# Optimization experiments

Hardware: AMD Instinct MI355X
Metric: run time of the kernel (lower is better)

Reference implementation:

```python
import jax, jax.numpy as jnp
import numpy as np

N = 50000       # num nodes
E = 600000      # num edges
IN = 128        # in_channels
H = 4           # heads
C = 32          # out_channels per head
B = 3           # num bends (Bezier control points)
NEG_SLOPE = 0.2


def setup_inputs() -> dict:
    key = jax.random.key(0)
    ks = jax.random.split(key, 6)
    x = jax.random.normal(ks[0], (N, IN), dtype=jnp.float32)
    edge_index = jax.random.randint(ks[1], (2, E), 0, N)
    # Bezier coefficients at t=0.5 for a 3-point curve: [0.25, 0.5, 0.25]
    coeffs_t = jnp.array([0.25, 0.5, 0.25], dtype=jnp.float32)
    glorot_w = float(np.sqrt(2.0) * np.sqrt(6.0 / (H * C + IN)))
    glorot_a = float(np.sqrt(2.0) * np.sqrt(6.0 / (1 + C)))
    lin_weight = jax.random.uniform(ks[2], (B, H * C, IN), jnp.float32, -glorot_w, glorot_w)
    lin_bias = jnp.zeros((B, H * C), dtype=jnp.float32)
    att_src = jax.random.uniform(ks[3], (B, 1, H, C), jnp.float32, -glorot_a, glorot_a)
    att_dst = jax.random.uniform(ks[4], (B, 1, H, C), jnp.float32, -glorot_a, glorot_a)
    return {"x": x, "edge_index": edge_index, "coeffs_t": coeffs_t,
            "lin_weight": lin_weight, "lin_bias": lin_bias,
            "att_src": att_src, "att_dst": att_dst}


def reference(x, edge_index, coeffs_t, lin_weight, lin_bias, att_src, att_dst):
    # Bezier parameter interpolation: weighted sum over bends
    W = jnp.einsum('b,boi->oi', coeffs_t, lin_weight)      # [H*C, IN]
    bias = jnp.einsum('b,bo->o', coeffs_t, lin_bias)       # [H*C]
    a_src = jnp.einsum('b,bqhc->qhc', coeffs_t, att_src)   # [1,H,C]
    a_dst = jnp.einsum('b,bqhc->qhc', coeffs_t, att_dst)   # [1,H,C]

    n = x.shape[0]
    xt = (x @ W.T + bias).reshape(n, H, C)                 # [N,H,C]
    alpha_src = jnp.sum(xt * a_src, axis=-1)               # [N,H]
    alpha_dst = jnp.sum(xt * a_dst, axis=-1)               # [N,H]

    row, col = edge_index[0], edge_index[1]
    alpha = alpha_src[row] + alpha_dst[col]                # [E,H]
    alpha = jax.nn.leaky_relu(alpha, NEG_SLOPE)

    # scatter-softmax over incoming edges of each target node (col)
    amax = jax.ops.segment_max(alpha, col, num_segments=n)  # [N,H]
    ex = jnp.exp(alpha - amax[col])                         # [E,H]
    denom = jax.ops.segment_sum(ex, col, num_segments=n)    # [N,H]
    alpha = ex / (denom[col] + 1e-16)                       # [E,H]

    # weighted neighbor aggregation (edge-parallel segment reduction)
    msg = xt[row] * alpha[..., None]                        # [E,H,C]
    out = jax.ops.segment_sum(msg, col, num_segments=n)     # [N,H,C]
    return out.reshape(n, H * C)                            # concat=True
```

## Files before the change

### kernel.cpp

```cpp
#include <hip/hip_runtime.h>
#include <hip/hip_bf16.h>

#define GAT_IN   128
#define GAT_OUT  128
#define GAT_H    4
#define GAT_C    32
#define NEG_SLOPE 0.2f
#define BUCKET   48
#define NB       196
#define CAP      4096
#define E_B      2048
#define EPTH     8

typedef __attribute__((ext_vector_type(8))) short bf16x8;
typedef __attribute__((ext_vector_type(4))) float f32x4;
union U4 { uint4 u; bf16x8 v; };

static __device__ __forceinline__ unsigned int pack_bf16(float lo, float hi) {
    __hip_bfloat16 a = __float2bfloat16(lo);
    __hip_bfloat16 b = __float2bfloat16(hi);
    unsigned short ua = *reinterpret_cast<unsigned short*>(&a);
    unsigned short ub = *reinterpret_cast<unsigned short*>(&b);
    return (unsigned int)ua | ((unsigned int)ub << 16);
}

__global__ __launch_bounds__(256) void interp_kernel(
    const float* __restrict__ coeffs,
    const float* __restrict__ lw,
    const float* __restrict__ lb,
    const float* __restrict__ asr,
    const float* __restrict__ ads,
    unsigned int* __restrict__ wfrag,
    float* __restrict__ biasc,
    float* __restrict__ asrc, float* __restrict__ adst,
    int* __restrict__ bucket_pos)
{
    int b = blockIdx.x, t = threadIdx.x;
    int i = b * 256 + t;
    float c0 = coeffs[0], c1 = coeffs[1], c2 = coeffs[2];
    int lane = (i >> 2) & 63;
    int nk   = i >> 8;
    int jw   = i & 3;
    int nt = nk >> 2, ks = nk & 3;
    int o = nt * 16 + (lane & 15);
    int k = ks * 32 + (lane >> 4) * 8 + jw * 2;
    int idx = o * 128 + k;
    float w0 = c0 * lw[idx]     + c1 * lw[16384 + idx]     + c2 * lw[32768 + idx];
    float w1 = c0 * lw[idx + 1] + c1 * lw[16384 + idx + 1] + c2 * lw[32768 + idx + 1];
    wfrag[i] = pack_bf16(w0, w1);
    if (b == 0) {
        if (t < 128) {
            biasc[t] = c0 * lb[t]  + c1 * lb[128 + t]  + c2 * lb[256 + t];
            asrc[t]  = c0 * asr[t] + c1 * asr[128 + t] + c2 * asr[256 + t];
            adst[t]  = c0 * ads[t] + c1 * ads[128 + t] + c2 * ads[256 + t];
        }
        if (t < NB) bucket_pos[t] = 0;
    }
}

__global__ __launch_bounds__(256) void pass1_kernel(
    const int* __restrict__ ei, int ne,
    int* __restrict__ bucket_pos,
    unsigned int* __restrict__ coarse)
{
    __shared__ int hist[NB], hist2[NB], gbase[NB];
    int tid = threadIdx.x;
    int b0  = blockIdx.x * E_B;

    for (int i = tid; i < NB; i += 256) { hist[i] = 0; hist2[i] = 0; }

    int rows[EPTH], cols[EPTH];
    #pragma unroll
    for (int i = 0; i < EPTH; ++i) {
        int e = b0 + i * 256 + tid;
        cols[i] = (e < ne) ? ei[ne + e] : -1;
    }
    #pragma unroll
    for (int i = 0; i < EPTH; ++i) {
        int e = b0 + i * 256 + tid;
        rows[i] = (e < ne) ? ei[e] : 0;
    }
    __syncthreads();

    #pragma unroll
    for (int i = 0; i < EPTH; ++i)
        if (cols[i] >= 0) atomicAdd(&hist[cols[i] >> 8], 1);
    __syncthreads();

    for (int i = tid; i < NB; i += 256)
        gbase[i] = hist[i] ? atomicAdd(&bucket_pos[i], hist[i]) : 0;
    __syncthreads();

    #pragma unroll
    for (int i = 0; i < EPTH; ++i) {
        if (cols[i] >= 0) {
            int bk  = cols[i] >> 8;
            int pos = gbase[bk] + atomicAdd(&hist2[bk], 1);
            if (pos < CAP)
                coarse[bk * CAP + pos] =
                    ((unsigned int)cols[i] << 16) | (unsigned int)rows[i];
        }
    }
}

__global__ __launch_bounds__(256) void pass2_kernel(
    const int* __restrict__ bucket_pos,
    const unsigned int* __restrict__ coarse,
    int* __restrict__ cnt,
    unsigned short* __restrict__ esrc,
    int n)
{
    __shared__ __align__(16) unsigned short st[256 * BUCKET];
    __shared__ int lcnt[256];
    int b = blockIdx.x, tid = threadIdx.x;
    lcnt[tid] = 0;
    __syncthreads();

    int cb = bucket_pos[b]; if (cb > CAP) cb = CAP;
    const uint4* cq = (const uint4*)(coarse + (size_t)b * CAP);
    for (int base = tid * 4; base < cb; base += 1024) {
        uint4 v4 = cq[base >> 2];
        unsigned int vv[4] = {v4.x, v4.y, v4.z, v4.w};
        #pragma unroll
        for (int j = 0; j < 4; ++j) {
            if (base + j < cb) {
                unsigned int v = vv[j];
                int lc  = (int)(v >> 16) & 255;
                int pos = atomicAdd(&lcnt[lc], 1);
                if (pos < BUCKET)
                    st[lc * BUCKET + pos] = (unsigned short)(v & 0xFFFFu);
            }
        }
    }
    __syncthreads();

    int nodes = n - b * 256; if (nodes > 256) nodes = 256;
    if (tid < nodes) cnt[b * 256 + tid] = lcnt[tid];
    int nq = nodes * 6;
    uint4* dst = (uint4*)(esrc + (size_t)b * 256 * BUCKET);
    const uint4* src = (const uint4*)st;
    for (int i = tid; i < nq; i += 256) dst[i] = src[i];
}

__global__ __launch_bounds__(256) void gemm_alpha_kernel(
    const float* __restrict__ x,
    const unsigned int* __restrict__ wfrag,
    const float* __restrict__ biasc,
    const float* __restrict__ asrc,
    const float* __restrict__ adst,
    unsigned int* __restrict__ xtb,
    float* __restrict__ alpha_src,
    float* __restrict__ alpha_dst,
    int n)
{
    __shared__ __align__(16) float C[64 * 132];
    int tid  = threadIdx.x;
    int lane = tid & 63;
    int wave = tid >> 6;
    int quad = lane >> 4;
    int lm   = lane & 15;
    int m0   = blockIdx.x * 64 + wave * 16;

    f32x4 acc[8];
    #pragma unroll
    for (int t = 0; t < 8; ++t) acc[t] = (f32x4){0.f, 0.f, 0.f, 0.f};

    int arow = m0 + lm; if (arow >= n) arow = n - 1;
    const float4* xr = (const float4*)(x + (size_t)arow * 128 + quad * 8);
    const uint4*  wf = (const uint4*)wfrag;

    #pragma unroll
    for (int ks = 0; ks < 4; ++ks) {
        float4 a0 = xr[ks * 8 + 0];
        float4 a1 = xr[ks * 8 + 1];
        U4 af;
        af.u.x = pack_bf16(a0.x, a0.y);
        af.u.y = pack_bf16(a0.z, a0.w);
        af.u.z = pack_bf16(a1.x, a1.y);
        af.u.w = pack_bf16(a1.z, a1.w);
        #pragma unroll
        for (int nt = 0; nt < 8; ++nt) {
            U4 bf; bf.u = wf[(nt * 4 + ks) * 64 + lane];
            acc[nt] = __builtin_amdgcn_mfma_f32_16x16x32_bf16(
                af.v, bf.v, acc[nt], 0, 0, 0);
        }
    }

    #pragma unroll
    for (int nt = 0; nt < 8; ++nt) {
        int col = nt * 16 + lm;
        #pragma unroll
        for (int r = 0; r < 4; ++r) {
            int rowl = wave * 16 + quad * 4 + r;
            C[rowl * 132 + col] = acc[nt][r];
        }
    }
    __syncthreads();

    int rowl = wave * 16 + (lane >> 2);
    int seg  = lane & 3;
    int mrow = blockIdx.x * 64 + rowl;
    if (mrow < n) {
        const float4* cb = (const float4*)(C + rowl * 132 + seg * 32);
        const float4* bb = (const float4*)(biasc + seg * 32);
        const float4* sb = (const float4*)(asrc + seg * 32);
        const float4* db = (const float4*)(adst + seg * 32);
        float s = 0.f, d = 0.f;
        unsigned int ow[16];
        #pragma unroll
        for (int q = 0; q < 8; ++q) {
            float4 v = cb[q];
            float4 b = bb[q];
            v.x += b.x; v.y += b.y; v.z += b.z; v.w += b.w;
            float4 as = sb[q], ad = db[q];
            s += v.x * as.x + v.y * as.y + v.z * as.z + v.w * as.w;
            d += v.x * ad.x + v.y * ad.y + v.z * ad.z + v.w * ad.w;
            ow[q * 2 + 0] = pack_bf16(v.x, v.y);
            ow[q * 2 + 1] = pack_bf16(v.z, v.w);
        }
        alpha_src[mrow * 4 + seg] = s;
        alpha_dst[mrow * 4 + seg] = d;
        uint4* xo = (uint4*)(xtb + (size_t)mrow * 64 + seg * 16);
        #pragma unroll
        for (int q4 = 0; q4 < 4; ++q4)
            xo[q4] = make_uint4(ow[q4 * 4], ow[q4 * 4 + 1],
                                ow[q4 * 4 + 2], ow[q4 * 4 + 3]);
    }
}

static __device__ __forceinline__ void window16(
    uint4 qa, uint4 qb, int rem,
    unsigned int h, unsigned int sl, float ad,
    const unsigned int* __restrict__ xtb,
    const float* __restrict__ alpha_src,
    float& den, float4& acc)
{
    unsigned int w[8] = {qa.x, qa.y, qa.z, qa.w, qb.x, qb.y, qb.z, qb.w};
    int r[16];
    #pragma unroll
    for (int t = 0; t < 16; ++t) {
        unsigned int rr = (t & 1) ? (w[t >> 1] >> 16) : (w[t >> 1] & 0xFFFFu);
        r[t] = (t < rem) ? (int)rr : 0;
    }

    float as[16];
    #pragma unroll
    for (int t = 0; t < 16; ++t)
        as[t] = alpha_src[(((unsigned)r[t]) << 2) | h];
    uint2 u[16];
    #pragma unroll
    for (int t = 0; t < 16; ++t)
        u[t] = *(const uint2*)(xtb + ((((unsigned)r[t]) << 6) + (sl << 1)));

    float e[16];
    #pragma unroll
    for (int t = 0; t < 16; ++t) {
        float a = as[t] + ad;
        a = fmaxf(a, NEG_SLOPE * a);
        float ex = __expf(a);
        e[t] = (t < rem) ? ex : 0.f;
    }
    float s01 = e[0]+e[1],   s23 = e[2]+e[3],   s45 = e[4]+e[5],   s67 = e[6]+e[7];
    float s89 = e[8]+e[9],   sab = e[10]+e[11], scd = e[12]+e[13], sef = e[14]+e[15];
    den += ((s01+s23) + (s45+s67)) + ((s89+sab) + (scd+sef));

    #pragma unroll
    for (int t = 0; t < 16; ++t) {
        acc.x = fmaf(e[t], __uint_as_float(u[t].x << 16),          acc.x);
        acc.y = fmaf(e[t], __uint_as_float(u[t].x & 0xFFFF0000u),  acc.y);
        acc.z = fmaf(e[t], __uint_as_float(u[t].y << 16),          acc.z);
        acc.w = fmaf(e[t], __uint_as_float(u[t].y & 0xFFFF0000u),  acc.w);
    }
}

__global__ __launch_bounds__(256) void agg_kernel(
    const int* __restrict__ cnt,
    const unsigned short* __restrict__ esrc,
    const unsigned int* __restrict__ xtb,
    const float* __restrict__ alpha_src,
    const float* __restrict__ alpha_dst,
    float* __restrict__ out,
    int n)
{
    int wave = threadIdx.x >> 6;
    unsigned int lane = threadIdx.x & 63;
    unsigned int sub = lane >> 5;
    unsigned int sl  = lane & 31;
    int node = blockIdx.x * 8 + wave * 2 + (int)sub;
    bool active = node < n;
    int nodec = active ? node : 0;
    unsigned int h = sl >> 3;

    const uint4* ebq = (const uint4*)(esrc + (unsigned)nodec * BUCKET);
    uint4 qa = ebq[0];
    uint4 qb = ebq[1];
    int   m  = cnt[nodec];
    float ad = alpha_dst[((unsigned)nodec << 2) | h];
    if (!active) m = 0;
    if (m > BUCKET) m = BUCKET;

    float4 acc = make_float4(0.f, 0.f, 0.f, 0.f);
    float den = 0.f;

    window16(qa, qb, m, h, sl, ad, xtb, alpha_src, den, acc);

    for (int j = 16; j < m; j += 16) {
        int q = j >> 3;
        uint4 wa = ebq[q], wb = ebq[q + 1];
        window16(wa, wb, m - j, h, sl, ad, xtb, alpha_src, den, acc);
    }

    if (active) {
        float inv = 1.0f / (den + 1e-16f);
        ((float4*)out)[((unsigned)node << 5) | sl] =
            make_float4(acc.x * inv, acc.y * inv, acc.z * inv, acc.w * inv);
    }
}

extern "C" void kernel_launch(void* const* d_in, const int* in_sizes, int n_in,
                              void* d_out, int out_size, void* d_ws, size_t ws_size,
                              hipStream_t stream)
{
    const float* x      = (const float*)d_in[0];
    const int*   ei     = (const int*)  d_in[1];
    const float* coeffs = (const float*)d_in[2];
    const float* lw     = (const float*)d_in[3];
    const float* lb     = (const float*)d_in[4];
    const float* asr    = (const float*)d_in[5];
    const float* ads    = (const float*)d_in[6];
    float* out = (float*)d_out;

    int n  = in_sizes[0] / GAT_IN;
    int ne = in_sizes[1] / 2;

    float* ws        = (float*)d_ws;
    unsigned int* wfrag = (unsigned int*)ws;
    float* biasc     = ws + 16384;
    float* asrc      = ws + 16512;
    float* adst      = ws + 16640;
    unsigned int* xtb = (unsigned int*)(ws + 16768);
    float* alpha_src = (float*)(xtb + (size_t)n * 64);
    float* alpha_dst = alpha_src + (size_t)n * 4;
    int*   cnt       = (int*)(alpha_dst + (size_t)n * 4);
    int*   bucket_pos = cnt + n;
    unsigned int* coarse = (unsigned int*)(bucket_pos + 256);
    unsigned short* esrc = (unsigned short*)(coarse + (size_t)NB * CAP);

    interp_kernel<<<32, 256, 0, stream>>>(
        coeffs, lw, lb, asr, ads, wfrag, biasc, asrc, adst, bucket_pos);
    pass1_kernel<<<(ne + E_B - 1) / E_B, 256, 0, stream>>>(
        ei, ne, bucket_pos, coarse);
    pass2_kernel<<<NB, 256, 0, stream>>>(bucket_pos, coarse, cnt, esrc, n);
    gemm_alpha_kernel<<<(n + 63) / 64, 256, 0, stream>>>(
        x, wfrag, biasc, asrc, adst, xtb, alpha_src, alpha_dst, n);
    agg_kernel<<<(n + 7) / 8, 256, 0, stream>>>(
        cnt, esrc, xtb, alpha_src, alpha_dst, out, n);
}
```

Baseline: 151.5 us.

## Fuse edge-bucketing pass1 and GEMM into one horizontally-fused launch

Combines the independent edge bucketing pass and the node GEMM/alpha kernel into one grid, where blocks are dispatched by index to one role or the other, sharing a union shared-memory buffer. This removes one kernel launch and lets the memory-bound scatter work overlap with the MFMA GEMM work on the GPU. The fused kernel's shared memory is sized for the GEMM, which may lower occupancy for the pass1 blocks.

```diff
diff --git a/kernel.cpp b/kernel.cpp
--- a/kernel.cpp
+++ b/kernel.cpp
@@ -58,14 +58,14 @@
     }
 }
 
-__global__ __launch_bounds__(256) void pass1_kernel(
+static __device__ __forceinline__ void pass1_body(
+    int blk, int* hist, int* hist2, int* gbase,
     const int* __restrict__ ei, int ne,
     int* __restrict__ bucket_pos,
     unsigned int* __restrict__ coarse)
 {
-    __shared__ int hist[NB], hist2[NB], gbase[NB];
     int tid = threadIdx.x;
-    int b0  = blockIdx.x * E_B;
+    int b0  = blk * E_B;
 
     for (int i = tid; i < NB; i += 256) { hist[i] = 0; hist2[i] = 0; }
 
@@ -103,46 +103,8 @@
     }
 }
 
-__global__ __launch_bounds__(256) void pass2_kernel(
-    const int* __restrict__ bucket_pos,
-    const unsigned int* __restrict__ coarse,
-    int* __restrict__ cnt,
-    unsigned short* __restrict__ esrc,
-    int n)
-{
-    __shared__ __align__(16) unsigned short st[256 * BUCKET];
-    __shared__ int lcnt[256];
-    int b = blockIdx.x, tid = threadIdx.x;
-    lcnt[tid] = 0;
-    __syncthreads();
-
-    int cb = bucket_pos[b]; if (cb > CAP) cb = CAP;
-    const uint4* cq = (const uint4*)(coarse + (size_t)b * CAP);
-    for (int base = tid * 4; base < cb; base += 1024) {
-        uint4 v4 = cq[base >> 2];
-        unsigned int vv[4] = {v4.x, v4.y, v4.z, v4.w};
-        #pragma unroll
-        for (int j = 0; j < 4; ++j) {
-            if (base + j < cb) {
-                unsigned int v = vv[j];
-                int lc  = (int)(v >> 16) & 255;
-                int pos = atomicAdd(&lcnt[lc], 1);
-                if (pos < BUCKET)
-                    st[lc * BUCKET + pos] = (unsigned short)(v & 0xFFFFu);
-            }
-        }
-    }
-    __syncthreads();
-
-    int nodes = n - b * 256; if (nodes > 256) nodes = 256;
-    if (tid < nodes) cnt[b * 256 + tid] = lcnt[tid];
-    int nq = nodes * 6;
-    uint4* dst = (uint4*)(esrc + (size_t)b * 256 * BUCKET);
-    const uint4* src = (const uint4*)st;
-    for (int i = tid; i < nq; i += 256) dst[i] = src[i];
-}
-
-__global__ __launch_bounds__(256) void gemm_alpha_kernel(
+static __device__ __forceinline__ void gemm_body(
+    int bu, float* C,
     const float* __restrict__ x,
     const unsigned int* __restrict__ wfrag,
     const float* __restrict__ biasc,
@@ -153,13 +115,12 @@
     float* __restrict__ alpha_dst,
     int n)
 {
-    __shared__ __align__(16) float C[64 * 132];
     int tid  = threadIdx.x;
     int lane = tid & 63;
     int wave = tid >> 6;
     int quad = lane >> 4;
     int lm   = lane & 15;
-    int m0   = blockIdx.x * 64 + wave * 16;
+    int m0   = bu * 64 + wave * 16;
 
     f32x4 acc[8];
     #pragma unroll
@@ -199,7 +160,7 @@
 
     int rowl = wave * 16 + (lane >> 2);
     int seg  = lane & 3;
-    int mrow = blockIdx.x * 64 + rowl;
+    int mrow = bu * 64 + rowl;
     if (mrow < n) {
         const float4* cb = (const float4*)(C + rowl * 132 + seg * 32);
         const float4* bb = (const float4*)(biasc + seg * 32);
@@ -226,6 +187,72 @@
             xo[q4] = make_uint4(ow[q4 * 4], ow[q4 * 4 + 1],
                                 ow[q4 * 4 + 2], ow[q4 * 4 + 3]);
     }
+}
+
+__global__ __launch_bounds__(256) void fused_p1_gemm_kernel(
+    const int* __restrict__ ei, int ne,
+    int* __restrict__ bucket_pos,
+    unsigned int* __restrict__ coarse,
+    const float* __restrict__ x,
+    const unsigned int* __restrict__ wfrag,
+    const float* __restrict__ biasc,
+    const float* __restrict__ asrc,
+    const float* __restrict__ adst,
+    unsigned int* __restrict__ xtb,
+    float* __restrict__ alpha_src,
+    float* __restrict__ alpha_dst,
+    int n, int p1b)
+{
+    __shared__ __align__(16) unsigned char smem[64 * 132 * 4];
+    int b = blockIdx.x;
+    if (b < p1b) {
+        int* hist  = (int*)smem;
+        int* hist2 = hist + NB;
+        int* gbase = hist2 + NB;
+        pass1_body(b, hist, hist2, gbase, ei, ne, bucket_pos, coarse);
+    } else {
+        gemm_body(b - p1b, (float*)smem, x, wfrag, biasc, asrc, adst,
+                  xtb, alpha_src, alpha_dst, n);
+    }
+}
+
+__global__ __launch_bounds__(256) void pass2_kernel(
+    const int* __restrict__ bucket_pos,
+    const unsigned int* __restrict__ coarse,
+    int* __restrict__ cnt,
+    unsigned short* __restrict__ esrc,
+    int n)
+{
+    __shared__ __align__(16) unsigned short st[256 * BUCKET];
+    __shared__ int lcnt[256];
+    int b = blockIdx.x, tid = threadIdx.x;
+    lcnt[tid] = 0;
+    __syncthreads();
+
+    int cb = bucket_pos[b]; if (cb > CAP) cb = CAP;
+    const uint4* cq = (const uint4*)(coarse + (size_t)b * CAP);
+    for (int base = tid * 4; base < cb; base += 1024) {
+        uint4 v4 = cq[base >> 2];
+        unsigned int vv[4] = {v4.x, v4.y, v4.z, v4.w};
+        #pragma unroll
+        for (int j = 0; j < 4; ++j) {
+            if (base + j < cb) {
+                unsigned int v = vv[j];
+                int lc  = (int)(v >> 16) & 255;
+                int pos = atomicAdd(&lcnt[lc], 1);
+                if (pos < BUCKET)
+                    st[lc * BUCKET + pos] = (unsigned short)(v & 0xFFFFu);
+            }
+        }
+    }
+    __syncthreads();
+
+    int nodes = n - b * 256; if (nodes > 256) nodes = 256;
+    if (tid < nodes) cnt[b * 256 + tid] = lcnt[tid];
+    int nq = nodes * 6;
+    uint4* dst = (uint4*)(esrc + (size_t)b * 256 * BUCKET);
+    const uint4* src = (const uint4*)st;
+    for (int i = tid; i < nq; i += 256) dst[i] = src[i];
 }
 
 static __device__ __forceinline__ void window16(
@@ -346,13 +373,15 @@
     unsigned int* coarse = (unsigned int*)(bucket_pos + 256);
     unsigned short* esrc = (unsigned short*)(coarse + (size_t)NB * CAP);
 
+    int p1b = (ne + E_B - 1) / E_B;
+    int gu  = (n + 63) / 64;
+
     interp_kernel<<<32, 256, 0, stream>>>(
         coeffs, lw, lb, asr, ads, wfrag, biasc, asrc, adst, bucket_pos);
-    pass1_kernel<<<(ne + E_B - 1) / E_B, 256, 0, stream>>>(
-        ei, ne, bucket_pos, coarse);
+    fused_p1_gemm_kernel<<<p1b + gu, 256, 0, stream>>>(
+        ei, ne, bucket_pos, coarse,
+        x, wfrag, biasc, asrc, adst, xtb, alpha_src, alpha_dst, n, p1b);
     pass2_kernel<<<NB, 256, 0, stream>>>(bucket_pos, coarse, cnt, esrc, n);
-    gemm_alpha_kernel<<<(n + 63) / 64, 256, 0, stream>>>(
-        x, wfrag, biasc, asrc, adst, xtb, alpha_src, alpha_dst, n);
     agg_kernel<<<(n + 7) / 8, 256, 0, stream>>>(
         cnt, esrc, xtb, alpha_src, alpha_dst, out, n);
 }
```

Result: faster. 146.5 us (-3.3%).
